# Kernel tuning notes

Hardware: AMD Instinct MI355X
Metric: run time of the kernel (lower is better)

## Reference

```python
import jax, jax.numpy as jnp
import numpy as np

N_HEADS = 16

def setup_inputs() -> dict:
    key = jax.random.key(0)
    ks = jax.random.split(key, 9)
    B, L, D = 4, 2048, 1024
    s = D ** -0.5
    return {
        "x": jax.random.normal(ks[0], (B, L, D), dtype=jnp.float32),
        "Wq": jax.random.normal(ks[1], (D, D), dtype=jnp.float32) * s,
        "bq": jax.random.normal(ks[2], (D,), dtype=jnp.float32) * 0.02,
        "Wk": jax.random.normal(ks[3], (D, D), dtype=jnp.float32) * s,
        "bk": jax.random.normal(ks[4], (D,), dtype=jnp.float32) * 0.02,
        "Wv": jax.random.normal(ks[5], (D, D), dtype=jnp.float32) * s,
        "bv": jax.random.normal(ks[6], (D,), dtype=jnp.float32) * 0.02,
        "Wo": jax.random.normal(ks[7], (D, D), dtype=jnp.float32) * s,
        "bo": jax.random.normal(ks[8], (D,), dtype=jnp.float32) * 0.02,
    }

def reference(x, Wq, bq, Wk, bk, Wv, bv, Wo, bo):
    B, L, D = x.shape
    H = N_HEADS
    hd = D // H
    scale = hd ** -0.5
    # torch Linear: y = x @ W.T + b
    q = (x @ Wq.T + bq).reshape(B, L, H, hd)
    k = (x @ Wk.T + bk).reshape(B, L, H, hd)
    v = (x @ Wv.T + bv).reshape(B, L, H, hd)
    # scores [B,H,L,L]
    qk = jnp.einsum('bqhd,bkhd->bhqk', q, k) * scale
    causal = jnp.tril(jnp.ones((L, L), dtype=bool))
    qk = jnp.where(causal[None, None, :, :], qk, -jnp.inf)
    attn = jax.nn.softmax(qk, axis=-1)
    out = jnp.einsum('bhqk,bkhd->bqhd', attn, v).reshape(B, L, D)
    return out @ Wo.T + bo
```

## Files before the change

### kernel.cpp

```cpp
#include <hip/hip_runtime.h>
#include <hip/hip_bf16.h>
#include <math.h>

#define Bsz 4
#define Lsz 2048
#define Dsz 1024
#define Hn 16
#define HDsz 64

typedef __attribute__((ext_vector_type(8))) short short8;
typedef __attribute__((ext_vector_type(4))) short short4_t;
typedef __attribute__((ext_vector_type(4))) float floatx4;
typedef unsigned short ushort_t;

__device__ __forceinline__ void load_lds_16B(const void* g, void* l) {
    __builtin_amdgcn_global_load_lds(
        (const __attribute__((address_space(1))) unsigned int*)g,
        (__attribute__((address_space(3))) unsigned int*)l, 16, 0, 0);
}

__device__ inline void cvt_store(float* p, size_t i, float v) { p[i] = v; }
__device__ inline void cvt_store(__hip_bfloat16* p, size_t i, float v) {
    p[i] = __float2bfloat16(v);
}

__device__ inline ushort_t f2bf_raw(float f) {
    __hip_bfloat16 b = __float2bfloat16(f);
    return *reinterpret_cast<ushort_t*>(&b);
}

__global__ __launch_bounds__(256) void f2b(const float* __restrict__ in,
                                           __hip_bfloat16* __restrict__ out,
                                           int n) {
    int i = (blockIdx.x * 256 + threadIdx.x) * 4;
    if (i >= n) return;
    float4 v = *(const float4*)(in + i);
    out[i + 0] = __float2bfloat16(v.x);
    out[i + 1] = __float2bfloat16(v.y);
    out[i + 2] = __float2bfloat16(v.z);
    out[i + 3] = __float2bfloat16(v.w);
}

template <typename TO, bool QKV>
__global__ __launch_bounds__(256) void gemm_bt_mfma(
    const ushort_t* __restrict__ A, const ushort_t* __restrict__ W,
    const float* __restrict__ b0, const float* __restrict__ b1,
    const float* __restrict__ b2, TO* __restrict__ C, int M, int N, int K) {
    __shared__ ushort_t As[128 * 32];
    __shared__ ushort_t Bs[128 * 32];

    const int t = threadIdx.x;
    const int wave = t >> 6, lane = t & 63;
    const int m0 = blockIdx.y * 128, n0 = blockIdx.x * 128;
    const int wm = (wave & 1) * 64, wn = (wave >> 1) * 64;
    const int lmod = lane & 15, quad = lane >> 4;

    floatx4 acc[4][4] = {};

    for (int k0 = 0; k0 < K; k0 += 32) {
#pragma unroll
        for (int p = 0; p < 2; p++) {
            int chunk = t + p * 256;
            int r = chunk >> 2;
            int c8 = (chunk & 3) * 8;
            load_lds_16B(A + (size_t)(m0 + r) * K + k0 + c8, &As[chunk * 8]);
            load_lds_16B(W + (size_t)(n0 + r) * K + k0 + c8, &Bs[chunk * 8]);
        }
        __syncthreads();

        short8 af[4], bf_[4];
#pragma unroll
        for (int i = 0; i < 4; i++) {
            af[i] = *(const short8*)&As[(wm + i * 16 + lmod) * 32 + quad * 8];
            bf_[i] = *(const short8*)&Bs[(wn + i * 16 + lmod) * 32 + quad * 8];
        }
#pragma unroll
        for (int i = 0; i < 4; i++)
#pragma unroll
            for (int j = 0; j < 4; j++)
                acc[i][j] = __builtin_amdgcn_mfma_f32_16x16x32_bf16(
                    af[i], bf_[j], acc[i][j], 0, 0, 0);
        __syncthreads();
    }

    const int sec = n0 >> 10;
    const float* bp = QKV ? (sec == 0 ? b0 : (sec == 1 ? b1 : b2)) : b0;
    TO* Cb = QKV ? (C + (size_t)sec * M * 1024) : C;
    const int Nout = QKV ? 1024 : N;

#pragma unroll
    for (int i = 0; i < 4; i++) {
        int gm = m0 + wm + i * 16 + quad * 4;
#pragma unroll
        for (int j = 0; j < 4; j++) {
            int gn = n0 + wn + j * 16 + lmod;
            int cn = QKV ? (gn & 1023) : gn;
            float b = bp[cn];
#pragma unroll
            for (int r = 0; r < 4; r++)
                cvt_store(Cb, (size_t)(gm + r) * Nout + cn, acc[i][j][r] + b);
        }
    }
}

__global__ __launch_bounds__(256) void attn_mfma(
    const ushort_t* __restrict__ q, const ushort_t* __restrict__ k,
    const ushort_t* __restrict__ v, ushort_t* __restrict__ ao) {
    __shared__ ushort_t Ks[64 * 64];
    __shared__ ushort_t Vts[64 * 64];
    __shared__ ushort_t Ps[4][32 * 64];

    const int t = threadIdx.x;
    const int wave = t >> 6, lane = t & 63;
    const int lmod = lane & 15, quad = lane >> 4;
    const int pair = blockIdx.x;
    const int bh = blockIdx.y;
    const int b = bh >> 4, h = bh & 15;
    const size_t base = ((size_t)b * Lsz) * Dsz + h * HDsz;

    const int vrp = t & 31, vcg = t >> 5;
    ushort_t* Pw = (ushort_t*)Ps[wave];
    const int lm7 = lmod & 7;
    const float SC2 = 0.1803368801111204f;

#pragma unroll 1
    for (int seg = 0; seg < 2; seg++) {
        const int qtile = seg == 0 ? (Lsz / 128 - 1 - pair) : pair;
        const int q0 = qtile * 128;

        short8 aq[2][2];
#pragma unroll
        for (int g = 0; g < 2; g++) {
            const ushort_t* qp = q + base +
                                 (size_t)(q0 + wave * 32 + g * 16 + lmod) * Dsz +
                                 quad * 8;
            aq[g][0] = *(const short8*)(qp);
            aq[g][1] = *(const short8*)(qp + 32);
        }

        floatx4 Oacc[2][4] = {};
        float lsum[2] = {0.f, 0.f};

        const int last_kt = 2 * qtile + 1;
        for (int kt = 0; kt <= last_kt; kt++) {
            __syncthreads();

#pragma unroll
            for (int p = 0; p < 2; p++) {
                int slot = t + p * 256;
                int row = slot >> 3, c8 = slot & 7;
                int gc8 = c8 ^ (row & 7);
                load_lds_16B(k + base + (size_t)(kt * 64 + row) * Dsz + gc8 * 8,
                             &Ks[slot * 8]);
            }
            {
                const ushort_t* v0p =
                    v + base + (size_t)(kt * 64 + 2 * vrp) * Dsz + vcg * 8;
                short8 v0 = *(const short8*)v0p;
                short8 v1 = *(const short8*)(v0p + Dsz);
                const int kk = 2 * vrp;
                const int kc8 = kk >> 3, klo = kk & 7;
#pragma unroll
                for (int j = 0; j < 8; j++) {
                    int d = vcg * 8 + j;
                    int sc8 = kc8 ^ (d & 7);
                    unsigned int pk = (unsigned int)(unsigned short)v0[j] |
                                      ((unsigned int)(unsigned short)v1[j] << 16);
                    *(unsigned int*)&Vts[d * 64 + sc8 * 8 + klo] = pk;
                }
            }
            __syncthreads();

            floatx4 St[2][4] = {};
#pragma unroll
            for (int nt = 0; nt < 4; nt++) {
                int key = nt * 16 + lmod;
#pragma unroll
                for (int ks = 0; ks < 2; ks++) {
                    int sc8 = (ks * 4 + quad) ^ (key & 7);
                    short8 kf = *(const short8*)&Ks[(key * 8 + sc8) * 8];
#pragma unroll
                    for (int g = 0; g < 2; g++)
                        St[g][nt] = __builtin_amdgcn_mfma_f32_16x16x32_bf16(
                            kf, aq[g][ks], St[g][nt], 0, 0, 0);
                }
            }

            const bool need_mask = (kt >= 2 * qtile);
#pragma unroll
            for (int g = 0; g < 2; g++) {
                int qg = q0 + wave * 32 + g * 16 + lmod;
#pragma unroll
                for (int nt = 0; nt < 4; nt++) {
                    int k0g = kt * 64 + nt * 16 + quad * 4;
                    short4_t pk;
#pragma unroll
                    for (int r = 0; r < 4; r++) {
                        float p = exp2f(St[g][nt][r] * SC2);
                        if (need_mask && (k0g + r > qg)) p = 0.f;
                        lsum[g] += p;
                        pk[r] = (short)f2bf_raw(p);
                    }
                    int c8 = nt * 2 + (quad >> 1);
                    int sc8 = c8 ^ lm7;
                    *(short4_t*)&Pw[((g * 16 + lmod) * 8 + sc8) * 8 +
                                    (quad & 1) * 4] = pk;
                }
            }

            short8 ap[2][2];
#pragma unroll
            for (int g = 0; g < 2; g++)
#pragma unroll
                for (int ks = 0; ks < 2; ks++) {
                    int sc8 = (ks * 4 + quad) ^ lm7;
                    ap[g][ks] =
                        *(const short8*)&Pw[((g * 16 + lmod) * 8 + sc8) * 8];
                }
#pragma unroll
            for (int on = 0; on < 4; on++) {
                int d = on * 16 + lmod;
#pragma unroll
                for (int ks = 0; ks < 2; ks++) {
                    int sc8 = (ks * 4 + quad) ^ (d & 7);
                    short8 bv = *(const short8*)&Vts[(d * 8 + sc8) * 8];
#pragma unroll
                    for (int g = 0; g < 2; g++)
                        Oacc[g][on] = __builtin_amdgcn_mfma_f32_16x16x32_bf16(
                            ap[g][ks], bv, Oacc[g][on], 0, 0, 0);
                }
            }
        }

#pragma unroll
        for (int g = 0; g < 2; g++) {
            lsum[g] += __shfl_xor(lsum[g], 16);
            lsum[g] += __shfl_xor(lsum[g], 32);
        }

#pragma unroll
        for (int g = 0; g < 2; g++) {
#pragma unroll
            for (int r = 0; r < 4; r++) {
                float lq = __shfl(lsum[g], quad * 4 + r);
                float inv = 1.0f / lq;
                int qg = q0 + wave * 32 + g * 16 + quad * 4 + r;
#pragma unroll
                for (int on = 0; on < 4; on++) {
                    int d = on * 16 + lmod;
                    ao[base + (size_t)qg * Dsz + d] =
                        f2bf_raw(Oacc[g][on][r] * inv);
                }
            }
        }
    }
}

extern "C" void kernel_launch(void* const* d_in, const int* in_sizes, int n_in,
                              void* d_out, int out_size, void* d_ws,
                              size_t ws_size, hipStream_t stream) {
    const size_t elems = (size_t)Bsz * Lsz * Dsz;
    const size_t welem = (size_t)Dsz * Dsz;
    if (ws_size < (5 * elems + 4 * welem) * sizeof(__hip_bfloat16)) return;

    const float* x = (const float*)d_in[0];
    const float* Wq = (const float*)d_in[1];
    const float* bq = (const float*)d_in[2];
    const float* Wk = (const float*)d_in[3];
    const float* bk = (const float*)d_in[4];
    const float* Wv = (const float*)d_in[5];
    const float* bv = (const float*)d_in[6];
    const float* Wo = (const float*)d_in[7];
    const float* bo = (const float*)d_in[8];
    float* out = (float*)d_out;

    __hip_bfloat16* xb = (__hip_bfloat16*)d_ws;
    __hip_bfloat16* q = xb + elems;
    __hip_bfloat16* k = q + elems;
    __hip_bfloat16* v = k + elems;
    __hip_bfloat16* ao = v + elems;
    __hip_bfloat16* Wqb = ao + elems;
    __hip_bfloat16* Wkb = Wqb + welem;
    __hip_bfloat16* Wvb = Wkb + welem;
    __hip_bfloat16* Wob = Wvb + welem;

    const int M = Bsz * Lsz, N = Dsz, K = Dsz;

    f2b<<<(int)(elems / 4 + 255) / 256, 256, 0, stream>>>(x, xb, (int)elems);
    f2b<<<(int)(welem / 4 + 255) / 256, 256, 0, stream>>>(Wq, Wqb, (int)welem);
    f2b<<<(int)(welem / 4 + 255) / 256, 256, 0, stream>>>(Wk, Wkb, (int)welem);
    f2b<<<(int)(welem / 4 + 255) / 256, 256, 0, stream>>>(Wv, Wvb, (int)welem);
    f2b<<<(int)(welem / 4 + 255) / 256, 256, 0, stream>>>(Wo, Wob, (int)welem);

    gemm_bt_mfma<__hip_bfloat16, true><<<dim3(3 * N / 128, M / 128), 256, 0,
                                         stream>>>(
        (const ushort_t*)xb, (const ushort_t*)Wqb, bq, bk, bv, q, M, 3 * N, K);

    attn_mfma<<<dim3(8, Bsz * Hn), 256, 0, stream>>>(
        (const ushort_t*)q, (const ushort_t*)k, (const ushort_t*)v,
        (ushort_t*)ao);

    gemm_bt_mfma<float, false><<<dim3(N / 128, M / 128), 256, 0, stream>>>(
        (const ushort_t*)ao, (const ushort_t*)Wob, bo, bo, bo, out, M, N, K);
}
```

Before: 306.8 us.

## Split attention key range in two and merge partials in a combine kernel

Each causal query-tile pair is now processed by two blocks, and each block handles half of the key tiles. The attention grid therefore doubles from 512 to 1024 blocks, which is meant to raise occupancy and latency hiding across the CUs. Each block writes an unnormalized bf16 partial output and its row sums to the workspace. A new combine kernel adds the two partials and normalizes them into the attention output. The cost is an extra kernel launch, roughly 32 MB of additional partial-result traffic, and rounding the partial accumulators to bf16 before they are combined.

After: 318.5 us. +3.8%, slower.

```diff
diff --git a/kernel.cpp b/kernel.cpp
--- a/kernel.cpp
+++ b/kernel.cpp
@@ -7,6 +7,7 @@
 #define Dsz 1024
 #define Hn 16
 #define HDsz 64
+#define NQT 16
 
 typedef __attribute__((ext_vector_type(8))) short short8;
 typedef __attribute__((ext_vector_type(4))) short short4_t;
@@ -27,6 +28,12 @@
 __device__ inline ushort_t f2bf_raw(float f) {
     __hip_bfloat16 b = __float2bfloat16(f);
     return *reinterpret_cast<ushort_t*>(&b);
+}
+
+__device__ inline float bf2f_raw(ushort_t u) {
+    union { unsigned int i; float f; } c;
+    c.i = ((unsigned int)u) << 16;
+    return c.f;
 }
 
 __global__ __launch_bounds__(256) void f2b(const float* __restrict__ in,
@@ -105,7 +112,8 @@
 
 __global__ __launch_bounds__(256) void attn_mfma(
     const ushort_t* __restrict__ q, const ushort_t* __restrict__ k,
-    const ushort_t* __restrict__ v, ushort_t* __restrict__ ao) {
+    const ushort_t* __restrict__ v, ushort_t* __restrict__ Opart,
+    float* __restrict__ lpart) {
     __shared__ ushort_t Ks[64 * 64];
     __shared__ ushort_t Vts[64 * 64];
     __shared__ ushort_t Ps[4][32 * 64];
@@ -113,7 +121,7 @@
     const int t = threadIdx.x;
     const int wave = t >> 6, lane = t & 63;
     const int lmod = lane & 15, quad = lane >> 4;
-    const int pair = blockIdx.x;
+    const int p = blockIdx.x & 7, s = blockIdx.x >> 3;
     const int bh = blockIdx.y;
     const int b = bh >> 4, h = bh & 15;
     const size_t base = ((size_t)b * Lsz) * Dsz + h * HDsz;
@@ -125,8 +133,10 @@
 
 #pragma unroll 1
     for (int seg = 0; seg < 2; seg++) {
-        const int qtile = seg == 0 ? (Lsz / 128 - 1 - pair) : pair;
+        const int qtile = seg == 0 ? (NQT - 1 - p) : p;
         const int q0 = qtile * 128;
+        const int Th = qtile + 1;
+        const int kt0 = s * Th, kt1 = kt0 + Th;
 
         short8 aq[2][2];
 #pragma unroll
@@ -141,13 +151,12 @@
         floatx4 Oacc[2][4] = {};
         float lsum[2] = {0.f, 0.f};
 
-        const int last_kt = 2 * qtile + 1;
-        for (int kt = 0; kt <= last_kt; kt++) {
+        for (int kt = kt0; kt < kt1; kt++) {
             __syncthreads();
 
 #pragma unroll
-            for (int p = 0; p < 2; p++) {
-                int slot = t + p * 256;
+            for (int pp = 0; pp < 2; pp++) {
+                int slot = t + pp * 256;
                 int row = slot >> 3, c8 = slot & 7;
                 int gc8 = c8 ^ (row & 7);
                 load_lds_16B(k + base + (size_t)(kt * 64 + row) * Dsz + gc8 * 8,
@@ -196,10 +205,10 @@
                     short4_t pk;
 #pragma unroll
                     for (int r = 0; r < 4; r++) {
-                        float p = exp2f(St[g][nt][r] * SC2);
-                        if (need_mask && (k0g + r > qg)) p = 0.f;
-                        lsum[g] += p;
-                        pk[r] = (short)f2bf_raw(p);
+                        float pe = exp2f(St[g][nt][r] * SC2);
+                        if (need_mask && (k0g + r > qg)) pe = 0.f;
+                        lsum[g] += pe;
+                        pk[r] = (short)f2bf_raw(pe);
                     }
                     int c8 = nt * 2 + (quad >> 1);
                     int sc8 = c8 ^ lm7;
@@ -238,22 +247,52 @@
             lsum[g] += __shfl_xor(lsum[g], 32);
         }
 
+        const size_t rec = ((size_t)bh * NQT + qtile) * 2 + s;
+        ushort_t* Orec = Opart + rec * (128 * 64);
+        float* lrec = lpart + rec * 128;
 #pragma unroll
         for (int g = 0; g < 2; g++) {
+            if (quad == 0) lrec[wave * 32 + g * 16 + lmod] = lsum[g];
 #pragma unroll
             for (int r = 0; r < 4; r++) {
-                float lq = __shfl(lsum[g], quad * 4 + r);
-                float inv = 1.0f / lq;
-                int qg = q0 + wave * 32 + g * 16 + quad * 4 + r;
+                int row = wave * 32 + g * 16 + quad * 4 + r;
 #pragma unroll
                 for (int on = 0; on < 4; on++) {
                     int d = on * 16 + lmod;
-                    ao[base + (size_t)qg * Dsz + d] =
-                        f2bf_raw(Oacc[g][on][r] * inv);
+                    Orec[row * 64 + d] = f2bf_raw(Oacc[g][on][r]);
                 }
             }
         }
     }
+}
+
+__global__ __launch_bounds__(256) void attn_combine(
+    const ushort_t* __restrict__ Opart, const float* __restrict__ lpart,
+    ushort_t* __restrict__ ao) {
+    int gidx = blockIdx.x * 256 + threadIdx.x;
+    int rowglob = gidx >> 3;
+    int c8 = (gidx & 7) * 8;
+    int bh = rowglob >> 11;
+    int r11 = rowglob & 2047;
+    int qtile = r11 >> 7, row = r11 & 127;
+
+    size_t rec0 = (((size_t)bh * NQT + qtile) * 2) * 1;
+    const ushort_t* O0 = Opart + (rec0 + 0) * (128 * 64) + row * 64 + c8;
+    const ushort_t* O1 = Opart + (rec0 + 1) * (128 * 64) + row * 64 + c8;
+    float l = lpart[(rec0 + 0) * 128 + row] + lpart[(rec0 + 1) * 128 + row];
+    float inv = 1.0f / l;
+
+    short8 a = *(const short8*)O0;
+    short8 bvec = *(const short8*)O1;
+    short8 o;
+#pragma unroll
+    for (int j = 0; j < 8; j++) {
+        float vv = (bf2f_raw((ushort_t)a[j]) + bf2f_raw((ushort_t)bvec[j])) * inv;
+        o[j] = (short)f2bf_raw(vv);
+    }
+    int b = bh >> 4, h = bh & 15;
+    int qg = qtile * 128 + row;
+    *(short8*)&ao[((size_t)(b * Lsz + qg)) * Dsz + h * HDsz + c8] = o;
 }
 
 extern "C" void kernel_launch(void* const* d_in, const int* in_sizes, int n_in,
@@ -261,7 +300,10 @@
                               size_t ws_size, hipStream_t stream) {
     const size_t elems = (size_t)Bsz * Lsz * Dsz;
     const size_t welem = (size_t)Dsz * Dsz;
-    if (ws_size < (5 * elems + 4 * welem) * sizeof(__hip_bfloat16)) return;
+    const size_t nrec = (size_t)Bsz * Hn * NQT * 2;
+    const size_t opart_e = nrec * 128 * 64;
+    const size_t need = (5 * elems + 4 * welem + opart_e) * 2 + nrec * 128 * 4;
+    if (ws_size < need) return;
 
     const float* x = (const float*)d_in[0];
     const float* Wq = (const float*)d_in[1];
@@ -283,6 +325,8 @@
     __hip_bfloat16* Wkb = Wqb + welem;
     __hip_bfloat16* Wvb = Wkb + welem;
     __hip_bfloat16* Wob = Wvb + welem;
+    ushort_t* Opart = (ushort_t*)(Wob + welem);
+    float* lpart = (float*)(Opart + opart_e);
 
     const int M = Bsz * Lsz, N = Dsz, K = Dsz;
 
@@ -296,9 +340,12 @@
                                          stream>>>(
         (const ushort_t*)xb, (const ushort_t*)Wqb, bq, bk, bv, q, M, 3 * N, K);
 
-    attn_mfma<<<dim3(8, Bsz * Hn), 256, 0, stream>>>(
-        (const ushort_t*)q, (const ushort_t*)k, (const ushort_t*)v,
-        (ushort_t*)ao);
+    attn_mfma<<<dim3(16, Bsz * Hn), 256, 0, stream>>>(
+        (const ushort_t*)q, (const ushort_t*)k, (const ushort_t*)v, Opart,
+        lpart);
+
+    attn_combine<<<(int)(elems / 8 / 256), 256, 0, stream>>>(Opart, lpart,
+                                                             (ushort_t*)ao);
 
     gemm_bt_mfma<float, false><<<dim3(N / 128, M / 128), 256, 0, stream>>>(
         (const ushort_t*)ao, (const ushort_t*)Wob, bo, bo, bo, out, M, N, K);
```
